# Performance work log

Hardware: AMD Instinct MI355X
Metric: run time of the kernel (lower is better)

Reference implementation:

```python
import jax, jax.numpy as jnp
import numpy as np

W_SEG = 2048   # segment_length w
R = 4          # dilation r
H = 16         # num_attention_heads


def setup_inputs() -> dict:
    key = jax.random.key(0)
    k0, k1, k2 = jax.random.split(key, 3)
    B, S, Hid = 2, 8192, 1024
    X = jax.random.normal(k0, (B, S, Hid), dtype=jnp.float32)
    Wq = jax.random.normal(k1, (Hid, Hid), dtype=jnp.float32) * 0.02
    bq = jnp.zeros((Hid,), jnp.float32)
    Wkv = jax.random.normal(k2, (Hid, 2 * Hid), dtype=jnp.float32) * 0.02
    bkv = jnp.zeros((2 * Hid,), jnp.float32)
    return {"X": X, "Wq": Wq, "bq": bq, "Wkv": Wkv, "bkv": bkv}


def reference(X, Wq, bq, Wkv, bkv):
    B, S, Hid = X.shape
    D = Hid // H                      # head dim
    num_points = W_SEG // R           # tokens kept per segment
    num_seg = S // W_SEG
    scale = 1.0 / np.sqrt(D).astype(np.float32)

    q = (X @ Wq + bq).reshape(B, S, H, D)
    kv = (X @ Wkv + bkv).reshape(B, S, 2, H, D)
    k, v = kv[:, :, 0], kv[:, :, 1]

    # dilated base indices: segment offset + r-strided points -> [num_seg*num_points]
    base = (jnp.arange(num_seg)[:, None] * W_SEG
            + jnp.arange(num_points)[None, :] * R).reshape(-1)
    shift = jnp.arange(H) % R                       # per-head shift
    idx = base[None, :] + shift[:, None]            # [H, T']
    Tq = idx.shape[1]
    idxT = idx.T                                    # [T', H]
    head_ix = jnp.arange(H)[None, :]                # [1, H] -> broadcasts with idxT

    # per-head dilated gather: sparse[b, t, h, d] = full[b, idx[h, t], h, d]
    sq = q[:, idxT, head_ix, :]                     # [B, T', H, D]
    sk = k[:, idxT, head_ix, :]
    sv = v[:, idxT, head_ix, :]

    sq = sq.reshape(B, num_seg, num_points, H, D)
    sk = sk.reshape(B, num_seg, num_points, H, D)
    sv = sv.reshape(B, num_seg, num_points, H, D)

    # per-segment (non-causal) attention, same math as flash_attn_kvpacked_func
    scores = jnp.einsum('bsqhd,bskhd->bshqk', sq, sk) * scale
    probs = jax.nn.softmax(scores, axis=-1)
    ctx = jnp.einsum('bshqk,bskhd->bsqhd', probs, sv)
    ctx = ctx.reshape(B, Tq, H, D)

    # scatter back into zeros at the gathered positions (unique per head)
    out = jnp.zeros((B, S, H, D), ctx.dtype).at[:, idxT, head_ix, :].set(ctx)
    return out.reshape(B, S, Hid)
```

## Files before the change

kernel.cpp:

```cpp
#include <hip/hip_runtime.h>

typedef unsigned short u16;
typedef unsigned int   u32;
typedef __bf16 bf16x8 __attribute__((ext_vector_type(8)));
typedef float  f32x4  __attribute__((ext_vector_type(4)));
typedef short  s16x4  __attribute__((ext_vector_type(4)));

#define QSCALE 0.125f

__device__ __forceinline__ u16 f2bf(float f) {
  union { float f; u32 u; } a; a.f = f;
  u32 u = a.u;
  u = (u + 0x7FFFu + ((u >> 16) & 1u)) >> 16;
  return (u16)u;
}

__device__ __forceinline__ u32 pack2bf(float a, float b) {
  u32 xa = __float_as_uint(a) + 0x8000u;
  u32 xb = __float_as_uint(b) + 0x8000u;
  return __builtin_amdgcn_perm(xb, xa, 0x07060302u);
}

__device__ __forceinline__ void async16(const void* g, void* l) {
  __builtin_amdgcn_global_load_lds(
      (const __attribute__((address_space(1))) void*)g,
      (__attribute__((address_space(3))) void*)l, 16, 0, 0);
}

__global__ __launch_bounds__(256) void pack(const float* __restrict__ X,
                                            u16* __restrict__ Xp,
                                            const float* __restrict__ Wq,
                                            const float* __restrict__ Wkv,
                                            u16* __restrict__ Wp,
                                            const float* __restrict__ bq,
                                            const float* __restrict__ bkv,
                                            float* __restrict__ bp) {
  __shared__ float tile[32][65];
  __shared__ u16 sh[4096];
  int bx = blockIdx.x;
  int tid = threadIdx.x;
  if (bx < 4096) {
    int ks = bx & 31, Mtile = (bx >> 5) & 31, r = bx >> 10;
    int rl = tid >> 1, half = tid & 1;
    int mt = rl >> 4, mm = rl & 15;
    int srow = (Mtile >> 2) * 2048 + ((Mtile & 3) * 128 + rl) * 4 + r;
    const float* s0 = X + (size_t)srow * 1024 + ks * 32 + half * 16;
    float4 a0 = *(const float4*)(s0);
    float4 a1 = *(const float4*)(s0 + 4);
    float4 a2 = *(const float4*)(s0 + 8);
    float4 a3 = *(const float4*)(s0 + 12);
    uint4 c0, c1;
    c0.x = pack2bf(a0.x, a0.y); c0.y = pack2bf(a0.z, a0.w);
    c0.z = pack2bf(a1.x, a1.y); c0.w = pack2bf(a1.z, a1.w);
    c1.x = pack2bf(a2.x, a2.y); c1.y = pack2bf(a2.z, a2.w);
    c1.z = pack2bf(a3.x, a3.y); c1.w = pack2bf(a3.z, a3.w);
    int base = (mt * 64 + mm) * 8 + half * 256;
    *(uint4*)&sh[base] = c0;
    *(uint4*)&sh[base + 128] = c1;
    __syncthreads();
    u16* dst = Xp + (size_t)bx * 4096 + tid * 16;
    uint4 d0 = *(const uint4*)&sh[tid * 16];
    uint4 d1 = *(const uint4*)&sh[tid * 16 + 8];
    *(uint4*)(dst) = d0;
    *(uint4*)(dst + 8) = d1;
    return;
  }
  int bw = bx - 4096;
  if (bw >= 1536) {
    int idx = (bw - 1536) * 256 + tid;
    int r = idx / 768, n = idx % 768;
    int t = n >> 8, hh = (n >> 6) & 3, d = n & 63;
    int h = hh * 4 + r;
    float v = (t == 0) ? bq[h * 64 + d] * QSCALE
            : (t == 1) ? bkv[h * 64 + d]
                       : bkv[1024 + h * 64 + d];
    bp[idx] = v;
    return;
  }
  int ks = bw & 31; int rem = bw >> 5;
  int hh = rem & 3; rem >>= 2;
  int t  = rem % 3; int r = rem / 3;
  int h  = hh * 4 + r;
  const float* src; int rs, cb;
  if (t == 0)      { src = Wq;  rs = 1024; cb = h * 64; }
  else if (t == 1) { src = Wkv; rs = 2048; cb = h * 64; }
  else             { src = Wkv; rs = 2048; cb = 1024 + h * 64; }
  {
    int kk = tid >> 3, dd = (tid & 7) << 3;
    const float* s0 = src + (size_t)(ks * 32 + kk) * rs + cb + dd;
    float4 a = *(const float4*)s0;
    float4 c = *(const float4*)(s0 + 4);
    tile[kk][dd + 0] = a.x; tile[kk][dd + 1] = a.y;
    tile[kk][dd + 2] = a.z; tile[kk][dd + 3] = a.w;
    tile[kk][dd + 4] = c.x; tile[kk][dd + 5] = c.y;
    tile[kk][dd + 6] = c.z; tile[kk][dd + 7] = c.w;
  }
  __syncthreads();
  {
    int d = tid >> 2, kc = tid & 3;
    float sc = (t == 0) ? QSCALE : 1.0f;
    u32 w[4];
#pragma unroll
    for (int j = 0; j < 4; ++j) {
      u16 lo = f2bf(tile[kc * 8 + 2 * j][d] * sc);
      u16 hi = f2bf(tile[kc * 8 + 2 * j + 1][d] * sc);
      w[j] = (u32)lo | ((u32)hi << 16);
    }
    int n = t * 256 + hh * 64 + d;
    int Nt = n >> 7, nt = (n >> 4) & 7, nn = n & 15;
    size_t off = (size_t)r * 786432 + (size_t)Nt * 131072 +
                 (size_t)ks * 4096 + nt * 512 + kc * 128 + nn * 8;
    uint4 o; o.x = w[0]; o.y = w[1]; o.z = w[2]; o.w = w[3];
    *(uint4*)(Wp + off) = o;
  }
}

__global__ __launch_bounds__(256, 3) void gemm1(const u16* __restrict__ Ap,
                                                const u16* __restrict__ Wp,
                                                const float* __restrict__ bp,
                                                u16* __restrict__ Qd,
                                                u16* __restrict__ Kd,
                                                u16* __restrict__ Vd) {
  __shared__ u16 lds[16384];
  u16* bufA0 = lds;
  u16* bufA1 = lds + 4096;
  u16* bufB0 = lds + 8192;
  u16* bufB1 = lds + 12288;
  int bx = blockIdx.x;
  int xcd = bx & 7;
  int idx = bx >> 3;
  int r = xcd >> 1;
  int Mtile = (xcd & 1) * 16 + (idx / 6);
  int Ntile = idx % 6;
  int tid = threadIdx.x, w = tid >> 6, lane = tid & 63;
  int wr = w >> 1, wc = w & 1;
  int l15 = lane & 15, l4 = lane >> 4;

  const u16* Aw = Ap + (size_t)(r * 32 + Mtile) * 131072 + w * 1024 + lane * 8;
  const u16* Bw = Wp + (size_t)r * 786432 + (size_t)Ntile * 131072 +
                  w * 1024 + lane * 8;

  async16(Aw,       &bufA0[w * 1024]);
  async16(Aw + 512, &bufA0[w * 1024 + 512]);
  async16(Bw,       &bufB0[w * 1024]);
  async16(Bw + 512, &bufB0[w * 1024 + 512]);

  f32x4 acc[4][4] = {};
  for (int ks = 0; ks < 32; ++ks) {
    u16* bA = (ks & 1) ? bufA1 : bufA0;
    u16* bB = (ks & 1) ? bufB1 : bufB0;
    __syncthreads();
    if (ks < 31) {
      u16* nA = (ks & 1) ? bufA0 : bufA1;
      u16* nB = (ks & 1) ? bufB0 : bufB1;
      const u16* a = Aw + (ks + 1) * 4096;
      const u16* b = Bw + (ks + 1) * 4096;
      async16(a,       &nA[w * 1024]);
      async16(a + 512, &nA[w * 1024 + 512]);
      async16(b,       &nB[w * 1024]);
      async16(b + 512, &nB[w * 1024 + 512]);
    }
    bf16x8 af[4], bf[4];
#pragma unroll
    for (int i = 0; i < 4; ++i)
      af[i] = *(const bf16x8*)&bA[((wr * 4 + i) * 64 + lane) * 8];
#pragma unroll
    for (int j = 0; j < 4; ++j)
      bf[j] = *(const bf16x8*)&bB[((wc * 4 + j) * 64 + lane) * 8];
#pragma unroll
    for (int i = 0; i < 4; ++i)
#pragma unroll
      for (int j = 0; j < 4; ++j)
        acc[i][j] = __builtin_amdgcn_mfma_f32_16x16x32_bf16(af[i], bf[j],
                                                            acc[i][j], 0, 0, 0);
  }

  int nb = Ntile * 128 + wc * 64;
  int t = nb >> 8, hh = (nb >> 6) & 3;
  int h = hh * 4 + r;
  float biasv[4];
#pragma unroll
  for (int j = 0; j < 4; ++j) biasv[j] = bp[r * 768 + nb + j * 16 + l15];

  if (t == 2) {
    u16* vb = lds + w * 4096;
    __syncthreads();
#pragma unroll
    for (int i = 0; i < 4; ++i) {
      int G = i * 2 + (l4 >> 1);
      int o = (l4 & 1) * 4;
#pragma unroll
      for (int j = 0; j < 4; ++j) {
        int dd = j * 16 + l15;
        int Gs = (G ^ (dd & 7)) * 8 + o;
        s16x4 ov;
        ov[0] = (short)f2bf(acc[i][j][0] + biasv[j]);
        ov[1] = (short)f2bf(acc[i][j][1] + biasv[j]);
        ov[2] = (short)f2bf(acc[i][j][2] + biasv[j]);
        ov[3] = (short)f2bf(acc[i][j][3] + biasv[j]);
        *(s16x4*)&vb[dd * 64 + Gs] = ov;
      }
    }
    int p0 = (Mtile * 128 + wr * 64) & 511;
    int bseg = (Mtile * 128) >> 9;
    size_t ub = (size_t)(bseg * 16 + h) * 32768;
    int row8 = lane >> 3, gsel = lane & 7;
#pragma unroll
    for (int rr2 = 0; rr2 < 8; ++rr2) {
      int dd = rr2 * 8 + row8;
      uint4 dv = *(const uint4*)&vb[dd * 64 + ((gsel ^ (dd & 7)) * 8)];
      *(uint4*)(Vd + ub + (size_t)dd * 512 + p0 + gsel * 8) = dv;
    }
    return;
  }

  u16* T = (t == 0) ? Qd : Kd;
  u16* eb = lds + w * 1152;
  int rrow = lane >> 2, seg = lane & 3;
  __syncthreads();
#pragma unroll
  for (int i = 0; i < 4; ++i) {
#pragma unroll
    for (int j = 0; j < 4; ++j)
#pragma unroll
      for (int reg = 0; reg < 4; ++reg)
        eb[(l4 * 4 + reg) * 72 + j * 16 + l15] = f2bf(acc[i][j][reg] + biasv[j]);
    uint4 d0 = *(const uint4*)&eb[rrow * 72 + seg * 16];
    uint4 d1 = *(const uint4*)&eb[rrow * 72 + seg * 16 + 8];
    int m = Mtile * 128 + wr * 64 + i * 16 + rrow;
    int bseg = m >> 9, p = m & 511;
    size_t off = ((size_t)(bseg * 16 + h) * 512 + p) * 64 + seg * 16;
    *(uint4*)(T + off) = d0;
    *(uint4*)(T + off + 8) = d1;
  }
}

__global__ __launch_bounds__(512, 4) void attn(const u16* __restrict__ Qd,
                                               const u16* __restrict__ Kd,
                                               const u16* __restrict__ Vd,
                                               float* __restrict__ out) {
  __shared__ u16 ldsK[128 * 72];
  __shared__ u16 ldsV[64 * 136];
  int bx = blockIdx.x;
  int unit = bx & 127, qq = bx >> 7;
  int b = unit >> 6, seg = (unit >> 4) & 3, h = unit & 15;
  int tid = threadIdx.x, w = tid >> 6, lane = tid & 63;
  int l15 = lane & 15, l4 = lane >> 4;
  const u16* Qu = Qd + (size_t)unit * 32768;
  const u16* Ku = Kd + (size_t)unit * 32768;
  const u16* Vu = Vd + (size_t)unit * 32768;

  int q0 = qq * 128 + w * 16;
  bf16x8 qf[2];
#pragma unroll
  for (int hf = 0; hf < 2; ++hf)
    qf[hf] = *(const bf16x8*)(Qu + (q0 + l15) * 64 + hf * 32 + l4 * 8);

  f32x4 O[4] = {};
  float lrun = 0.f;

  int c0 = tid, c1 = 512 + tid;
  int kp0 = c0 >> 3, kd0 = c0 & 7;
  int kp1 = c1 >> 3, kd1 = c1 & 7;
  int vr0 = c0 >> 4, vc0 = (c0 & 15) << 3;
  int vr1 = c1 >> 4, vc1 = (c1 & 15) << 3;

  uint4 kreg0 = *(const uint4*)(Ku + c0 * 8);
  uint4 kreg1 = *(const uint4*)(Ku + c1 * 8);
  uint4 vreg0 = *(const uint4*)(Vu + vr0 * 512 + vc0);
  uint4 vreg1 = *(const uint4*)(Vu + vr1 * 512 + vc1);

  for (int ch = 0; ch < 4; ++ch) {
    __syncthreads();
    *(uint4*)&ldsK[kp0 * 72 + kd0 * 8] = kreg0;
    *(uint4*)&ldsK[kp1 * 72 + kd1 * 8] = kreg1;
    *(uint4*)&ldsV[vr0 * 136 + vc0] = vreg0;
    *(uint4*)&ldsV[vr1 * 136 + vc1] = vreg1;
    __syncthreads();
    if (ch < 3) {
      const u16* Ksn = Ku + (ch + 1) * 8192;
      const u16* Vsn = Vu + (ch + 1) * 128;
      kreg0 = *(const uint4*)(Ksn + c0 * 8);
      kreg1 = *(const uint4*)(Ksn + c1 * 8);
      vreg0 = *(const uint4*)(Vsn + vr0 * 512 + vc0);
      vreg1 = *(const uint4*)(Vsn + vr1 * 512 + vc1);
    }

    float csum = 0.f;
    s16x4 pk[8];
#pragma unroll
    for (int kt = 0; kt < 8; ++kt) {
      bf16x8 a0 = *(const bf16x8*)&ldsK[(kt * 16 + l15) * 72 + l4 * 8];
      bf16x8 a1 = *(const bf16x8*)&ldsK[(kt * 16 + l15) * 72 + 32 + l4 * 8];
      f32x4 s = __builtin_amdgcn_mfma_f32_16x16x32_bf16(
          a0, qf[0], (f32x4){0.f, 0.f, 0.f, 0.f}, 0, 0, 0);
      s = __builtin_amdgcn_mfma_f32_16x16x32_bf16(a1, qf[1], s, 0, 0, 0);
      float e0 = __expf(s[0]);
      float e1 = __expf(s[1]);
      float e2 = __expf(s[2]);
      float e3 = __expf(s[3]);
      csum += (e0 + e1) + (e2 + e3);
      s16x4 pv;
      pv[0] = (short)(__float_as_uint(e0) >> 16);
      pv[1] = (short)(__float_as_uint(e1) >> 16);
      pv[2] = (short)(__float_as_uint(e2) >> 16);
      pv[3] = (short)(__float_as_uint(e3) >> 16);
      pk[kt] = pv;
    }
    csum += __shfl_xor(csum, 16, 64);
    csum += __shfl_xor(csum, 32, 64);
    lrun += csum;
#pragma unroll
    for (int kt = 0; kt < 8; ++kt)
#pragma unroll
      for (int dn = 0; dn < 4; ++dn) {
        s16x4 vb = *(const s16x4*)&ldsV[(dn * 16 + l15) * 136 + kt * 16 + l4 * 4];
        O[dn] = __builtin_amdgcn_mfma_f32_16x16x16bf16_1k(pk[kt], vb,
                                                          O[dn], 0, 0, 0);
      }
  }

  {
    float rl = __builtin_amdgcn_rcpf(lrun);
#pragma unroll
    for (int reg = 0; reg < 4; ++reg) {
      float rr = __shfl(rl, l4 * 4 + reg, 64);
      int p = q0 + l4 * 4 + reg;
      int spos = seg * 2048 + p * 4 + (h & 3);
      size_t base = ((size_t)(b * 8192 + spos)) * 1024 + h * 64 + l15;
#pragma unroll
      for (int dn = 0; dn < 4; ++dn)
        out[base + dn * 16] = O[dn][reg] * rr;
    }
  }

  {
    int row_i = bx * 32 + (tid >> 4);
    int sub = tid & 15;
    int rr = row_i & 3;
    float4 z = {0.f, 0.f, 0.f, 0.f};
    float* rowp = out + (size_t)row_i * 1024 + sub * 4;
#pragma unroll
    for (int hz = 0; hz < 16; ++hz) {
      if ((hz & 3) == rr) continue;
      *(float4*)(rowp + hz * 64) = z;
    }
  }
}

extern "C" void kernel_launch(void* const* d_in, const int* in_sizes, int n_in,
                              void* d_out, int out_size, void* d_ws, size_t ws_size,
                              hipStream_t stream) {
  (void)in_sizes; (void)n_in; (void)ws_size; (void)out_size;
  const float* X   = (const float*)d_in[0];
  const float* Wq  = (const float*)d_in[1];
  const float* bq  = (const float*)d_in[2];
  const float* Wkv = (const float*)d_in[3];
  const float* bkv = (const float*)d_in[4];
  float* out = (float*)d_out;
  char* ws = (char*)d_ws;
  u16*  Wp = (u16*)(ws);
  float* bp = (float*)(ws + 6291456);
  u16*  Qd = (u16*)(ws + 6303744);
  u16*  Kd = (u16*)(ws + 14692352);
  u16*  Vd = (u16*)(ws + 23080960);
  u16*  Xp = (u16*)d_out;

  pack  <<<5644, 256, 0, stream>>>(X, Xp, Wq, Wkv, Wp, bq, bkv, bp);
  gemm1 <<<768,  256, 0, stream>>>(Xp, Wp, bp, Qd, Kd, Vd);
  attn  <<<512,  512, 0, stream>>>(Qd, Kd, Vd, out);
}
```

Baseline: 176.7 us.

## Double-buffer K/V tiles in LDS with async global-to-LDS loads and XOR swizzle

Replaces the register-staged K/V prefetch (global load to VGPRs, then LDS store between two barriers) with direct async global-to-LDS loads into two ping-pong LDS buffers. Padded row strides are replaced by an XOR swizzle to avoid bank conflicts. This removes one barrier per chunk and the register round-trip, and overlaps the next chunk's load with compute. LDS use grows to 64KB per block, which may limit occupancy given launch bounds of 512 threads x 4 blocks.

```diff
diff --git a/kernel.cpp b/kernel.cpp
--- a/kernel.cpp
+++ b/kernel.cpp
@@ -239,8 +239,11 @@
                                                const u16* __restrict__ Kd,
                                                const u16* __restrict__ Vd,
                                                float* __restrict__ out) {
-  __shared__ u16 ldsK[128 * 72];
-  __shared__ u16 ldsV[64 * 136];
+  __shared__ u16 lds[32768];
+  u16* K0 = lds;
+  u16* V0 = lds + 8192;
+  u16* K1 = lds + 16384;
+  u16* V1 = lds + 24576;
   int bx = blockIdx.x;
   int unit = bx & 127, qq = bx >> 7;
   int b = unit >> 6, seg = (unit >> 4) & 3, h = unit & 15;
@@ -256,42 +259,45 @@
   for (int hf = 0; hf < 2; ++hf)
     qf[hf] = *(const bf16x8*)(Qu + (q0 + l15) * 64 + hf * 32 + l4 * 8);
 
+  const char* kS = (const char*)Ku + (w * 16 + (lane >> 3)) * 128 +
+                   (((lane & 7) ^ (lane >> 3)) * 16);
+  int dA = w * 8 + (lane >> 4);
+  int dB = dA + 4;
+  const char* vSA = (const char*)Vu + dA * 1024 + (((lane & 15) ^ (dA & 15)) * 16);
+  const char* vSB = (const char*)Vu + dB * 1024 + (((lane & 15) ^ (dB & 15)) * 16);
+
+#define STAGE_KV(KB, VB, ch) do {                                   \
+    async16(kS + (ch) * 16384,        (KB) + w * 1024);             \
+    async16(kS + (ch) * 16384 + 1024, (KB) + w * 1024 + 512);       \
+    async16(vSA + (ch) * 256,         (VB) + w * 1024);             \
+    async16(vSB + (ch) * 256,         (VB) + w * 1024 + 512);       \
+  } while (0)
+
+  STAGE_KV(K0, V0, 0);
+
   f32x4 O[4] = {};
   float lrun = 0.f;
-
-  int c0 = tid, c1 = 512 + tid;
-  int kp0 = c0 >> 3, kd0 = c0 & 7;
-  int kp1 = c1 >> 3, kd1 = c1 & 7;
-  int vr0 = c0 >> 4, vc0 = (c0 & 15) << 3;
-  int vr1 = c1 >> 4, vc1 = (c1 & 15) << 3;
-
-  uint4 kreg0 = *(const uint4*)(Ku + c0 * 8);
-  uint4 kreg1 = *(const uint4*)(Ku + c1 * 8);
-  uint4 vreg0 = *(const uint4*)(Vu + vr0 * 512 + vc0);
-  uint4 vreg1 = *(const uint4*)(Vu + vr1 * 512 + vc1);
+  int sx = l15 & 7;
+  int g0 = (l4 ^ sx) * 8;
+  int g1 = g0 ^ 32;
 
   for (int ch = 0; ch < 4; ++ch) {
-    __syncthreads();
-    *(uint4*)&ldsK[kp0 * 72 + kd0 * 8] = kreg0;
-    *(uint4*)&ldsK[kp1 * 72 + kd1 * 8] = kreg1;
-    *(uint4*)&ldsV[vr0 * 136 + vc0] = vreg0;
-    *(uint4*)&ldsV[vr1 * 136 + vc1] = vreg1;
+    u16* Kb = (ch & 1) ? K1 : K0;
+    u16* Vb = (ch & 1) ? V1 : V0;
     __syncthreads();
     if (ch < 3) {
-      const u16* Ksn = Ku + (ch + 1) * 8192;
-      const u16* Vsn = Vu + (ch + 1) * 128;
-      kreg0 = *(const uint4*)(Ksn + c0 * 8);
-      kreg1 = *(const uint4*)(Ksn + c1 * 8);
-      vreg0 = *(const uint4*)(Vsn + vr0 * 512 + vc0);
-      vreg1 = *(const uint4*)(Vsn + vr1 * 512 + vc1);
+      u16* nK = (ch & 1) ? K0 : K1;
+      u16* nV = (ch & 1) ? V0 : V1;
+      STAGE_KV(nK, nV, ch + 1);
     }
 
     float csum = 0.f;
     s16x4 pk[8];
 #pragma unroll
     for (int kt = 0; kt < 8; ++kt) {
-      bf16x8 a0 = *(const bf16x8*)&ldsK[(kt * 16 + l15) * 72 + l4 * 8];
-      bf16x8 a1 = *(const bf16x8*)&ldsK[(kt * 16 + l15) * 72 + 32 + l4 * 8];
+      const u16* krow = &Kb[(kt * 16 + l15) * 64];
+      bf16x8 a0 = *(const bf16x8*)&krow[g0];
+      bf16x8 a1 = *(const bf16x8*)&krow[g1];
       f32x4 s = __builtin_amdgcn_mfma_f32_16x16x32_bf16(
           a0, qf[0], (f32x4){0.f, 0.f, 0.f, 0.f}, 0, 0, 0);
       s = __builtin_amdgcn_mfma_f32_16x16x32_bf16(a1, qf[1], s, 0, 0, 0);
@@ -310,15 +316,19 @@
     csum += __shfl_xor(csum, 16, 64);
     csum += __shfl_xor(csum, 32, 64);
     lrun += csum;
-#pragma unroll
-    for (int kt = 0; kt < 8; ++kt)
+    int h2 = l4 >> 1, q4 = (l4 & 1) * 4;
+#pragma unroll
+    for (int kt = 0; kt < 8; ++kt) {
+      int gp = ((kt * 2 + h2) ^ l15) * 8 + q4;
 #pragma unroll
       for (int dn = 0; dn < 4; ++dn) {
-        s16x4 vb = *(const s16x4*)&ldsV[(dn * 16 + l15) * 136 + kt * 16 + l4 * 4];
+        s16x4 vb = *(const s16x4*)&Vb[(dn * 16 + l15) * 128 + gp];
         O[dn] = __builtin_amdgcn_mfma_f32_16x16x16bf16_1k(pk[kt], vb,
                                                           O[dn], 0, 0, 0);
       }
-  }
+    }
+  }
+#undef STAGE_KV
 
   {
     float rl = __builtin_amdgcn_rcpf(lrun);
```

After: 175.3 us (median of 2 runs). No clear change (-0.8%).
